# Performance work log

Measured on AMD Instinct MI355X. Metric: run time of the kernel, lower is better.

## Reference

```python
import jax, jax.numpy as jnp
import numpy as np

NUM_EMBEDDINGS = 512
EMBEDDING_DIM = 64
COMMITMENT_COST = 0.25


def setup_inputs() -> dict:
    key = jax.random.key(0)
    k1, k2 = jax.random.split(key)
    inputs = jax.random.normal(k1, (32, EMBEDDING_DIM, 64, 64), dtype=jnp.float32)  # NCHW
    # nn.Embedding weight init: uniform(-1/K, 1/K)
    embedding = jax.random.uniform(
        k2, (NUM_EMBEDDINGS, EMBEDDING_DIM), dtype=jnp.float32,
        minval=-1.0 / NUM_EMBEDDINGS, maxval=1.0 / NUM_EMBEDDINGS)
    return {"inputs": inputs, "embedding": embedding}


def reference(inputs, embedding):
    # NCHW -> NHWC, flatten to [N, D]
    x = jnp.transpose(inputs, (0, 2, 3, 1))
    flat = x.reshape(-1, EMBEDDING_DIM)  # [N, D]
    distances = (jnp.sum(flat * flat, axis=1, keepdims=True)
                 + jnp.sum(embedding * embedding, axis=1)
                 - 2.0 * flat @ embedding.T)
    idx = jnp.argmin(distances, axis=1)  # [N]
    # gather codebook rows (equivalent to one-hot @ embedding, fused)
    quantized = jnp.take(embedding, idx, axis=0).reshape(x.shape)
    e_latent_loss = jnp.mean((jax.lax.stop_gradient(quantized) - x) ** 2)
    q_latent_loss = jnp.mean((quantized - jax.lax.stop_gradient(x)) ** 2)
    loss = q_latent_loss + COMMITMENT_COST * e_latent_loss
    # straight-through estimator
    quantized = x + jax.lax.stop_gradient(quantized - x)
    out = jnp.transpose(quantized, (0, 3, 1, 2))  # back to NCHW
    return out, loss
```

## Files before the change

### kernel.cpp

```cpp
#include <hip/hip_runtime.h>


#define D 64
#define K_EMB 512
#define HW 4096
#define CHW (D * HW)
#define OUT_ELEMS 8388608
#define NB_MAIN 1024
#define SWZ(r) ((((r) ^ ((r) >> 2))) & 7)

typedef __attribute__((ext_vector_type(8))) short short8;
typedef __attribute__((ext_vector_type(4))) float f32x4;

__device__ __forceinline__ unsigned short f2bf(float f) {
    unsigned u = __float_as_uint(f);
    u += 0x7FFFu + ((u >> 16) & 1u);
    return (unsigned short)(u >> 16);
}
__device__ __forceinline__ float bf2f(unsigned short h) {
    return __uint_as_float(((unsigned)h) << 16);
}
__device__ __forceinline__ unsigned umin32(unsigned a, unsigned b) { return a <= b ? a : b; }

__global__ void vq_prep(const float* __restrict__ emb, unsigned short* __restrict__ ebf,
                        float* __restrict__ npm) {
    int k = blockIdx.x * 256 + threadIdx.x;
    const float4* e4 = reinterpret_cast<const float4*>(emb + k * D);
    unsigned short h[D];
    float acc = 0.f;
#pragma unroll
    for (int i = 0; i < 16; ++i) {
        float4 v = e4[i];
        acc += v.x * v.x + v.y * v.y + v.z * v.z + v.w * v.w;
        h[4 * i + 0] = f2bf(v.x); h[4 * i + 1] = f2bf(v.y);
        h[4 * i + 2] = f2bf(v.z); h[4 * i + 3] = f2bf(v.w);
    }
    npm[k] = -0.5f * (1.0f + acc);
    uint4* dst = reinterpret_cast<uint4*>(ebf + k * D);
#pragma unroll
    for (int i = 0; i < 8; ++i) {
        uint4 p;
        p.x = (unsigned)h[8 * i + 0] | ((unsigned)h[8 * i + 1] << 16);
        p.y = (unsigned)h[8 * i + 2] | ((unsigned)h[8 * i + 3] << 16);
        p.z = (unsigned)h[8 * i + 4] | ((unsigned)h[8 * i + 5] << 16);
        p.w = (unsigned)h[8 * i + 6] | ((unsigned)h[8 * i + 7] << 16);
        dst[i] = p;
    }
}

__global__ __launch_bounds__(256, 3) void vq_mfma(const float* __restrict__ in,
                                                  const unsigned short* __restrict__ ebf,
                                                  const float* __restrict__ npm,
                                                  const float* __restrict__ emb,
                                                  float* __restrict__ out,
                                                  float* __restrict__ partials) {
    __shared__ __align__(16) char ldsX[16384];
    __shared__ __align__(16) unsigned keysS[4][128];
    __shared__ float red4[4];

    const int tid = threadIdx.x;
    const int lane = tid & 63;
    const int w = tid >> 6;
    const int col = lane & 15;
    const int dg = lane >> 4;
    const int bid = ((blockIdx.x & 7) << 7) | (blockIdx.x >> 3);
    const int n = bid >> 5;
    const int hw0 = (bid & 31) << 7;

    {
        const int row = tid & 127;
        const int half = tid >> 7;
        const float* xb = in + n * CHW + hw0 + row;
#pragma unroll
        for (int cg = 0; cg < 4; ++cg) {
            const int cgi = half * 4 + cg;
            unsigned short h[8];
#pragma unroll
            for (int j = 0; j < 8; ++j) h[j] = f2bf(xb[(cgi * 8 + j) * HW]);
            uint4 p;
            p.x = (unsigned)h[0] | ((unsigned)h[1] << 16);
            p.y = (unsigned)h[2] | ((unsigned)h[3] << 16);
            p.z = (unsigned)h[4] | ((unsigned)h[5] << 16);
            p.w = (unsigned)h[6] | ((unsigned)h[7] << 16);
            *reinterpret_cast<uint4*>(ldsX + row * 128 + ((cgi ^ SWZ(row)) * 16)) = p;
        }
    }

    unsigned best[8][4];
#pragma unroll
    for (int rt = 0; rt < 8; ++rt)
#pragma unroll
        for (int i = 0; i < 4; ++i) best[rt][i] = 0xFFFFFFFFu;

    const short8* e8 = reinterpret_cast<const short8*>(ebf);
#pragma unroll 1
    for (int g = 0; g < 2; ++g) {
        const int kb = w * 128 + g * 64 + col;
        short8 ef[4][2];
        float npv[4];
#pragma unroll
        for (int ct = 0; ct < 4; ++ct) {
            const int k = kb + ct * 16;
            ef[ct][0] = e8[k * 8 + dg];
            ef[ct][1] = e8[k * 8 + 4 + dg];
            npv[ct] = npm[k];
        }
        if (g == 0) __syncthreads();

#pragma unroll
        for (int rt = 0; rt < 8; ++rt) {
            const int row = rt * 16 + col;
            short8 a0 = *reinterpret_cast<const short8*>(
                ldsX + row * 128 + ((dg ^ SWZ(row)) * 16));
            short8 a1 = *reinterpret_cast<const short8*>(
                ldsX + row * 128 + (((4 + dg) ^ SWZ(row)) * 16));
#pragma unroll
            for (int ct = 0; ct < 4; ++ct) {
                f32x4 acc = {npv[ct], npv[ct], npv[ct], npv[ct]};
                acc = __builtin_amdgcn_mfma_f32_16x16x32_bf16(a0, ef[ct][0], acc, 0, 0, 0);
                acc = __builtin_amdgcn_mfma_f32_16x16x32_bf16(a1, ef[ct][1], acc, 0, 0, 0);
                const unsigned kc = (unsigned)(kb + ct * 16);
#pragma unroll
                for (int i = 0; i < 4; ++i) {
                    unsigned key = (__float_as_uint(acc[i]) & 0xFFFFFE00u) | kc;
                    best[rt][i] = umin32(best[rt][i], key);
                }
            }
        }
    }

#pragma unroll
    for (int rt = 0; rt < 8; ++rt)
#pragma unroll
        for (int i = 0; i < 4; ++i) {
            unsigned k = best[rt][i];
#pragma unroll
            for (int s = 1; s < 16; s <<= 1)
                k = umin32(k, (unsigned)__shfl_xor((int)k, s, 64));
            if (col == 0) keysS[w][rt * 16 + dg * 4 + i] = k;
        }
    __syncthreads();

    const int rg = tid & 31;
    const int cs = tid >> 5;
    uint4 q0 = *reinterpret_cast<const uint4*>(&keysS[0][rg * 4]);
    uint4 q1 = *reinterpret_cast<const uint4*>(&keysS[1][rg * 4]);
    uint4 q2 = *reinterpret_cast<const uint4*>(&keysS[2][rg * 4]);
    uint4 q3 = *reinterpret_cast<const uint4*>(&keysS[3][rg * 4]);
    int kk[4];
    kk[0] = (int)(umin32(umin32(q0.x, q1.x), umin32(q2.x, q3.x)) & 511u);
    kk[1] = (int)(umin32(umin32(q0.y, q1.y), umin32(q2.y, q3.y)) & 511u);
    kk[2] = (int)(umin32(umin32(q0.z, q1.z), umin32(q2.z, q3.z)) & 511u);
    kk[3] = (int)(umin32(umin32(q0.w, q1.w), umin32(q2.w, q3.w)) & 511u);
    float ej[4][8];
#pragma unroll
    for (int j = 0; j < 4; ++j) {
        const f32x4* ep = reinterpret_cast<const f32x4*>(emb + kk[j] * D + cs * 8);
        *reinterpret_cast<f32x4*>(&ej[j][0]) = ep[0];
        *reinterpret_cast<f32x4*>(&ej[j][4]) = ep[1];
    }
    float lsum = 0.f;
#pragma unroll
    for (int j = 0; j < 4; ++j) {
        const int r = rg * 4 + j;
        short8 x8 = *reinterpret_cast<const short8*>(
            ldsX + r * 128 + ((cs ^ SWZ(r)) * 16));
#pragma unroll
        for (int t = 0; t < 8; ++t) {
            float d = ej[j][t] - bf2f((unsigned short)x8[t]);
            lsum = fmaf(d, d, lsum);
        }
    }
    float* obase = out + n * CHW + hw0 + rg * 4;
#pragma unroll
    for (int t = 0; t < 8; ++t) {
        f32x4 st = {ej[0][t], ej[1][t], ej[2][t], ej[3][t]};
        __builtin_nontemporal_store(st, reinterpret_cast<f32x4*>(obase + (cs * 8 + t) * HW));
    }

#pragma unroll
    for (int s = 1; s < 64; s <<= 1) lsum += __shfl_xor(lsum, s, 64);
    if (lane == 0) red4[w] = lsum;
    __syncthreads();
    if (tid == 0) partials[bid] = red4[0] + red4[1] + red4[2] + red4[3];
}

__global__ void vq_finalize(const float* __restrict__ partials, float* __restrict__ loss) {
    __shared__ float s[256];
    float a = 0.f;
    for (int i = threadIdx.x; i < NB_MAIN; i += 256) a += partials[i];
    s[threadIdx.x] = a;
    __syncthreads();
    for (int t = 128; t > 0; t >>= 1) {
        if ((int)threadIdx.x < t) s[threadIdx.x] += s[threadIdx.x + t];
        __syncthreads();
    }
    if (threadIdx.x == 0) loss[0] = 1.25f * s[0] * (1.0f / (float)OUT_ELEMS);
}

extern "C" void kernel_launch(void* const* d_in, const int* in_sizes, int n_in,
                              void* d_out, int out_size, void* d_ws, size_t ws_size,
                              hipStream_t stream) {
    const float* in = (const float*)d_in[0];
    const float* emb = (const float*)d_in[1];
    float* out = (float*)d_out;
    unsigned short* ebf = (unsigned short*)d_ws;
    float* npm = (float*)((char*)d_ws + 65536);
    float* partials = (float*)((char*)d_ws + 67584);

    vq_prep<<<2, 256, 0, stream>>>(emb, ebf, npm);
    vq_mfma<<<NB_MAIN, 256, 0, stream>>>(in, ebf, npm, emb, out, partials);
    vq_finalize<<<1, 256, 0, stream>>>(partials, out + OUT_ELEMS);
}
```

Measured before the change: 32.89 us.

## Fuse codebook prep into main kernel and vectorize input loads with packed bf16 convert

Removes the separate prep kernel: each block now reads the fp32 codebook directly, computes row norms with cross-lane shuffles, and converts to bf16 with the hardware packed-convert instruction. The input tile load is changed to 16-byte vector loads of 4 spatial positions per channel, converted with the packed bf16 instruction. Launch bounds are raised to 4 blocks per CU. This saves a kernel launch and a serial dependency, at the cost of every block redundantly re-reading the fp32 codebook (twice the bytes of the bf16 copy) and recomputing norms.

```diff
diff --git a/kernel.cpp b/kernel.cpp
--- a/kernel.cpp
+++ b/kernel.cpp
@@ -12,45 +12,17 @@
 typedef __attribute__((ext_vector_type(8))) short short8;
 typedef __attribute__((ext_vector_type(4))) float f32x4;
 
-__device__ __forceinline__ unsigned short f2bf(float f) {
-    unsigned u = __float_as_uint(f);
-    u += 0x7FFFu + ((u >> 16) & 1u);
-    return (unsigned short)(u >> 16);
-}
 __device__ __forceinline__ float bf2f(unsigned short h) {
     return __uint_as_float(((unsigned)h) << 16);
 }
 __device__ __forceinline__ unsigned umin32(unsigned a, unsigned b) { return a <= b ? a : b; }
-
-__global__ void vq_prep(const float* __restrict__ emb, unsigned short* __restrict__ ebf,
-                        float* __restrict__ npm) {
-    int k = blockIdx.x * 256 + threadIdx.x;
-    const float4* e4 = reinterpret_cast<const float4*>(emb + k * D);
-    unsigned short h[D];
-    float acc = 0.f;
-#pragma unroll
-    for (int i = 0; i < 16; ++i) {
-        float4 v = e4[i];
-        acc += v.x * v.x + v.y * v.y + v.z * v.z + v.w * v.w;
-        h[4 * i + 0] = f2bf(v.x); h[4 * i + 1] = f2bf(v.y);
-        h[4 * i + 2] = f2bf(v.z); h[4 * i + 3] = f2bf(v.w);
-    }
-    npm[k] = -0.5f * (1.0f + acc);
-    uint4* dst = reinterpret_cast<uint4*>(ebf + k * D);
-#pragma unroll
-    for (int i = 0; i < 8; ++i) {
-        uint4 p;
-        p.x = (unsigned)h[8 * i + 0] | ((unsigned)h[8 * i + 1] << 16);
-        p.y = (unsigned)h[8 * i + 2] | ((unsigned)h[8 * i + 3] << 16);
-        p.z = (unsigned)h[8 * i + 4] | ((unsigned)h[8 * i + 5] << 16);
-        p.w = (unsigned)h[8 * i + 6] | ((unsigned)h[8 * i + 7] << 16);
-        dst[i] = p;
-    }
-}
-
-__global__ __launch_bounds__(256, 3) void vq_mfma(const float* __restrict__ in,
-                                                  const unsigned short* __restrict__ ebf,
-                                                  const float* __restrict__ npm,
+__device__ __forceinline__ unsigned cvtpk(float lo, float hi) {
+    unsigned r;
+    asm("v_cvt_pk_bf16_f32 %0, %1, %2" : "=v"(r) : "v"(lo), "v"(hi));
+    return r;
+}
+
+__global__ __launch_bounds__(256, 4) void vq_mfma(const float* __restrict__ in,
                                                   const float* __restrict__ emb,
                                                   float* __restrict__ out,
                                                   float* __restrict__ partials) {
@@ -68,21 +40,22 @@
     const int hw0 = (bid & 31) << 7;
 
     {
-        const int row = tid & 127;
-        const int half = tid >> 7;
-        const float* xb = in + n * CHW + hw0 + row;
-#pragma unroll
-        for (int cg = 0; cg < 4; ++cg) {
-            const int cgi = half * 4 + cg;
-            unsigned short h[8];
-#pragma unroll
-            for (int j = 0; j < 8; ++j) h[j] = f2bf(xb[(cgi * 8 + j) * HW]);
+        const int rw = (tid & 31) * 4;
+        const int cg = tid >> 5;
+        const float* xb = in + n * CHW + cg * 8 * HW + hw0 + rw;
+        f32x4 v[8];
+#pragma unroll
+        for (int ch = 0; ch < 8; ++ch)
+            v[ch] = *reinterpret_cast<const f32x4*>(xb + ch * HW);
+#pragma unroll
+        for (int j = 0; j < 4; ++j) {
+            const int r = rw + j;
             uint4 p;
-            p.x = (unsigned)h[0] | ((unsigned)h[1] << 16);
-            p.y = (unsigned)h[2] | ((unsigned)h[3] << 16);
-            p.z = (unsigned)h[4] | ((unsigned)h[5] << 16);
-            p.w = (unsigned)h[6] | ((unsigned)h[7] << 16);
-            *reinterpret_cast<uint4*>(ldsX + row * 128 + ((cgi ^ SWZ(row)) * 16)) = p;
+            p.x = cvtpk(v[0][j], v[1][j]);
+            p.y = cvtpk(v[2][j], v[3][j]);
+            p.z = cvtpk(v[4][j], v[5][j]);
+            p.w = cvtpk(v[6][j], v[7][j]);
+            *reinterpret_cast<uint4*>(ldsX + r * 128 + ((cg ^ SWZ(r)) * 16)) = p;
         }
     }
 
@@ -92,7 +65,6 @@
 #pragma unroll
         for (int i = 0; i < 4; ++i) best[rt][i] = 0xFFFFFFFFu;
 
-    const short8* e8 = reinterpret_cast<const short8*>(ebf);
 #pragma unroll 1
     for (int g = 0; g < 2; ++g) {
         const int kb = w * 128 + g * 64 + col;
@@ -101,9 +73,27 @@
 #pragma unroll
         for (int ct = 0; ct < 4; ++ct) {
             const int k = kb + ct * 16;
-            ef[ct][0] = e8[k * 8 + dg];
-            ef[ct][1] = e8[k * 8 + 4 + dg];
-            npv[ct] = npm[k];
+            const float* ep = emb + k * D + dg * 8;
+            f32x4 a0 = *reinterpret_cast<const f32x4*>(ep);
+            f32x4 a1 = *reinterpret_cast<const f32x4*>(ep + 4);
+            f32x4 b0 = *reinterpret_cast<const f32x4*>(ep + 32);
+            f32x4 b1 = *reinterpret_cast<const f32x4*>(ep + 36);
+            float s = 0.f;
+#pragma unroll
+            for (int q = 0; q < 4; ++q) {
+                s = fmaf(a0[q], a0[q], s); s = fmaf(a1[q], a1[q], s);
+                s = fmaf(b0[q], b0[q], s); s = fmaf(b1[q], b1[q], s);
+            }
+            s += __shfl_xor(s, 16, 64);
+            s += __shfl_xor(s, 32, 64);
+            npv[ct] = -0.5f * (1.0f + s);
+            union { short8 s8; unsigned u[4]; } e0u, e1u;
+            e0u.u[0] = cvtpk(a0[0], a0[1]); e0u.u[1] = cvtpk(a0[2], a0[3]);
+            e0u.u[2] = cvtpk(a1[0], a1[1]); e0u.u[3] = cvtpk(a1[2], a1[3]);
+            e1u.u[0] = cvtpk(b0[0], b0[1]); e1u.u[1] = cvtpk(b0[2], b0[3]);
+            e1u.u[2] = cvtpk(b1[0], b1[1]); e1u.u[3] = cvtpk(b1[2], b1[3]);
+            ef[ct][0] = e0u.s8;
+            ef[ct][1] = e1u.s8;
         }
         if (g == 0) __syncthreads();
 
@@ -204,11 +194,8 @@
     const float* in = (const float*)d_in[0];
     const float* emb = (const float*)d_in[1];
     float* out = (float*)d_out;
-    unsigned short* ebf = (unsigned short*)d_ws;
-    float* npm = (float*)((char*)d_ws + 65536);
-    float* partials = (float*)((char*)d_ws + 67584);
-
-    vq_prep<<<2, 256, 0, stream>>>(emb, ebf, npm);
-    vq_mfma<<<NB_MAIN, 256, 0, stream>>>(in, ebf, npm, emb, out, partials);
+    float* partials = (float*)d_ws;
+
+    vq_mfma<<<NB_MAIN, 256, 0, stream>>>(in, emb, out, partials);
     vq_finalize<<<1, 256, 0, stream>>>(partials, out + OUT_ELEMS);
 }
```

Result: slower. 36.51 us (+11.0%).

## Vectorize input staging loads, use hardware bf16 pack, raise occupancy bound

Applied to the files above, without the earlier changes.

Input staging now has each thread load four consecutive spatial positions for eight channels as float4 vectors, replacing scalar strided loads. The fp32-to-bf16 conversion uses the v_cvt_pk_bf16_f32 instruction instead of a software rounding sequence. Launch bounds move from 3 to 4 waves per SIMD to allow more concurrent blocks. The aim is fewer load instructions, fewer ALU ops in the prologue and better latency hiding, at the risk of register spills under the tighter bound.

```diff
diff --git a/kernel.cpp b/kernel.cpp
--- a/kernel.cpp
+++ b/kernel.cpp
@@ -21,6 +21,11 @@
     return __uint_as_float(((unsigned)h) << 16);
 }
 __device__ __forceinline__ unsigned umin32(unsigned a, unsigned b) { return a <= b ? a : b; }
+__device__ __forceinline__ unsigned cvtpk(float lo, float hi) {
+    unsigned r;
+    asm("v_cvt_pk_bf16_f32 %0, %1, %2" : "=v"(r) : "v"(lo), "v"(hi));
+    return r;
+}
 
 __global__ void vq_prep(const float* __restrict__ emb, unsigned short* __restrict__ ebf,
                         float* __restrict__ npm) {
@@ -48,7 +53,7 @@
     }
 }
 
-__global__ __launch_bounds__(256, 3) void vq_mfma(const float* __restrict__ in,
+__global__ __launch_bounds__(256, 4) void vq_mfma(const float* __restrict__ in,
                                                   const unsigned short* __restrict__ ebf,
                                                   const float* __restrict__ npm,
                                                   const float* __restrict__ emb,
@@ -68,21 +73,22 @@
     const int hw0 = (bid & 31) << 7;
 
     {
-        const int row = tid & 127;
-        const int half = tid >> 7;
-        const float* xb = in + n * CHW + hw0 + row;
-#pragma unroll
-        for (int cg = 0; cg < 4; ++cg) {
-            const int cgi = half * 4 + cg;
-            unsigned short h[8];
-#pragma unroll
-            for (int j = 0; j < 8; ++j) h[j] = f2bf(xb[(cgi * 8 + j) * HW]);
+        const int rw = (tid & 31) * 4;
+        const int cg = tid >> 5;
+        const float* xb = in + n * CHW + cg * 8 * HW + hw0 + rw;
+        f32x4 v[8];
+#pragma unroll
+        for (int ch = 0; ch < 8; ++ch)
+            v[ch] = *reinterpret_cast<const f32x4*>(xb + ch * HW);
+#pragma unroll
+        for (int j = 0; j < 4; ++j) {
+            const int r = rw + j;
             uint4 p;
-            p.x = (unsigned)h[0] | ((unsigned)h[1] << 16);
-            p.y = (unsigned)h[2] | ((unsigned)h[3] << 16);
-            p.z = (unsigned)h[4] | ((unsigned)h[5] << 16);
-            p.w = (unsigned)h[6] | ((unsigned)h[7] << 16);
-            *reinterpret_cast<uint4*>(ldsX + row * 128 + ((cgi ^ SWZ(row)) * 16)) = p;
+            p.x = cvtpk(v[0][j], v[1][j]);
+            p.y = cvtpk(v[2][j], v[3][j]);
+            p.z = cvtpk(v[4][j], v[5][j]);
+            p.w = cvtpk(v[6][j], v[7][j]);
+            *reinterpret_cast<uint4*>(ldsX + r * 128 + ((cg ^ SWZ(r)) * 16)) = p;
         }
     }
 
```

Result: no change. 33.06 us (+0.5%).
